# Kernel tuning notes

Measured on AMD Instinct MI355X. Metric: run time of the kernel, lower is better.

## Reference

```python
import jax, jax.numpy as jnp
import numpy as np
import math

L, D_T, D, NL, NH, FFN, C, B = 24, 1024, 256, 12, 4, 1024, 2, 2048
HD = D // NH


def _layernorm(x, g, b, eps=1e-5):
    m = jnp.mean(x, axis=-1, keepdims=True)
    v = jnp.mean(jnp.square(x - m), axis=-1, keepdims=True)
    return (x - m) * jax.lax.rsqrt(v + eps) * g + b


def _rotate_half(x):
    x1, x2 = jnp.split(x, 2, axis=-1)
    return jnp.concatenate([-x2, x1], axis=-1)


def setup_inputs() -> dict:
    key = jax.random.key(0)
    ks = iter(jax.random.split(key, 64))
    n = lambda shape, s=0.02: jax.random.normal(next(ks), shape, dtype=jnp.float32) * s
    inp = {}
    inp['teacher_cls'] = jax.random.normal(next(ks), (B, L, D_T), dtype=jnp.float32)
    # input LN + projection
    inp['in_ln_g'] = jnp.ones((D_T,), jnp.float32); inp['in_ln_b'] = jnp.zeros((D_T,), jnp.float32)
    inp['proj_w'] = n((D, D_T)); inp['proj_b'] = jnp.zeros((D,), jnp.float32)
    # RoPE caches (buffers)
    inv_freq = 1.0 / (10000.0 ** (np.arange(0, D, 2, dtype=np.float32) / D))
    t = np.arange(L, dtype=np.float32)
    freqs = np.einsum('i,j->ij', t, inv_freq)
    emb = np.concatenate([freqs, freqs], axis=-1)
    inp['cos_cached'] = jnp.asarray(np.cos(emb)[None])  # [1,L,D]
    inp['sin_cached'] = jnp.asarray(np.sin(emb)[None])
    inp['pre_ln_g'] = jnp.ones((D,), jnp.float32); inp['pre_ln_b'] = jnp.zeros((D,), jnp.float32)
    # stacked transformer layer params [NL, ...]
    inp['l_ln1_g'] = jnp.ones((NL, D), jnp.float32); inp['l_ln1_b'] = jnp.zeros((NL, D), jnp.float32)
    inp['l_inw'] = n((NL, 3 * D, D)); inp['l_inb'] = jnp.zeros((NL, 3 * D), jnp.float32)
    inp['l_outw'] = n((NL, D, D)); inp['l_outb'] = jnp.zeros((NL, D), jnp.float32)
    inp['l_ln2_g'] = jnp.ones((NL, D), jnp.float32); inp['l_ln2_b'] = jnp.zeros((NL, D), jnp.float32)
    inp['l_w12'] = n((NL, 2 * FFN, D)); inp['l_b12'] = jnp.zeros((NL, 2 * FFN), jnp.float32)
    inp['l_w3'] = n((NL, D, FFN)); inp['l_b3'] = jnp.zeros((NL, D), jnp.float32)
    inp['post_ln_g'] = jnp.ones((D,), jnp.float32); inp['post_ln_b'] = jnp.zeros((D,), jnp.float32)
    # entropy gate
    inp['eg_w1'] = n((L, D, 8), 0.01); inp['eg_b1'] = jnp.zeros((L, 8), jnp.float32)
    inp['eg_w2'] = n((L, 8, 1), 0.01); inp['eg_b2'] = jnp.zeros((L, 1), jnp.float32)
    # per-position heads (stacked)
    inp['halt_w'] = n((L, D + 1)); inp['halt_b'] = jnp.full((L,), -4.0, jnp.float32)
    inp['cls_w'] = n((L, C, D)); inp['cls_b'] = jnp.zeros((L, C), jnp.float32)
    return inp


def _mha(x, inw, inb, outw, outb, mask):
    Bb, Ll, Dd = x.shape
    qkv = x @ inw.T + inb                              # [B,L,3D]
    q, k, v = jnp.split(qkv, 3, axis=-1)
    def heads(t):
        return t.reshape(Bb, Ll, NH, HD).transpose(0, 2, 1, 3)  # [B,H,L,hd]
    q, k, v = heads(q), heads(k), heads(v)
    scores = jnp.einsum('bhqd,bhkd->bhqk', q, k) / math.sqrt(HD)
    scores = jnp.where(mask, -jnp.inf, scores)
    attn = jax.nn.softmax(scores, axis=-1)
    o = jnp.einsum('bhqk,bhkd->bhqd', attn, v)
    o = o.transpose(0, 2, 1, 3).reshape(Bb, Ll, Dd)
    return o @ outw.T + outb


def reference(teacher_cls, in_ln_g, in_ln_b, proj_w, proj_b, cos_cached, sin_cached,
              pre_ln_g, pre_ln_b, l_ln1_g, l_ln1_b, l_inw, l_inb, l_outw, l_outb,
              l_ln2_g, l_ln2_b, l_w12, l_b12, l_w3, l_b3, post_ln_g, post_ln_b,
              eg_w1, eg_b1, eg_w2, eg_b2, halt_w, halt_b, cls_w, cls_b):
    x = _layernorm(teacher_cls, in_ln_g, in_ln_b)
    x = x @ proj_w.T + proj_b                          # [B,L,D]
    x = x * cos_cached + _rotate_half(x) * sin_cached  # RoPE
    z = _layernorm(x, pre_ln_g, pre_ln_b)
    mask = jnp.triu(jnp.ones((L, L), bool), 1)         # causal
    for i in range(NL):
        xn = _layernorm(z, l_ln1_g[i], l_ln1_b[i])
        z = z + _mha(xn, l_inw[i], l_inb[i], l_outw[i], l_outb[i], mask)
        xn = _layernorm(z, l_ln2_g[i], l_ln2_b[i])
        w12_out = xn @ l_w12[i].T + l_b12[i]           # [B,L,2*FFN]
        x1, x2 = jnp.split(w12_out, 2, axis=-1)
        hidden = jax.nn.silu(x1) * x2
        z = z + hidden @ l_w3[i].T + l_b3[i]
    z = _layernorm(z, post_ln_g, post_ln_b)
    # batched per-position classifier heads
    class_logits = jnp.einsum('bld,lcd->blc', z, cls_w) + cls_b   # [B,L,C]
    log_probs = jax.nn.log_softmax(class_logits, axis=-1)
    probs = jnp.exp(log_probs)
    probs_safe = jnp.clip(probs, 1e-10, 1.0)
    ent = -jnp.sum(probs_safe * jnp.log(probs_safe), axis=-1, keepdims=True)
    ent_norm = jnp.clip(ent / math.log(C), 0.0, 1.0)              # [B,L,1]
    # entropy gate
    h = jnp.tanh(jnp.einsum('bld,ldh->blh', z, eg_w1) + eg_b1)
    gate = jax.nn.sigmoid(jnp.einsum('blh,lho->blo', h, eg_w2) + eg_b2)
    gated = ent_norm * gate                                        # [B,L,1]
    # batched per-position halting heads
    combined = jnp.concatenate([z, gated], axis=-1)                # [B,L,D+1]
    halting_logits = jnp.einsum('bld,ld->bl', combined, halt_w) + halt_b
    return (halting_logits, class_logits, z)
```

## Files before the change

### kernel.cpp

```cpp
#include <hip/hip_runtime.h>
#include <hip/hip_bf16.h>
#include <math.h>

#define L_SEQ 24
#define DT 1024
#define DM 256
#define NLAYER 12
#define NHEAD 4
#define HDIM 64
#define FFND 1024
#define NCLS 2
#define NBATCH 2048
#define NTOK (NBATCH*L_SEQ)

typedef float f32x4 __attribute__((ext_vector_type(4)));
typedef __bf16 bf16x4 __attribute__((ext_vector_type(4)));
typedef __bf16 bf16x8 __attribute__((ext_vector_type(8)));

#define GLDS16(gp, lp) __builtin_amdgcn_global_load_lds((const __attribute__((address_space(1))) void*)(gp), (__attribute__((address_space(3))) void*)(lp), 16, 0, 0)
#define VMWAIT(N) asm volatile("s_waitcnt vmcnt(" #N ")" ::: "memory")
#define LGKM0()   asm volatile("s_waitcnt lgkmcnt(0)" ::: "memory")

__device__ inline float wred_sum(float v){
#pragma unroll
  for (int o = 32; o > 0; o >>= 1) v += __shfl_xor(v, o);
  return v;
}
__device__ inline float wred_max(float v){
#pragma unroll
  for (int o = 32; o > 0; o >>= 1) v = fmaxf(v, __shfl_xor(v, o));
  return v;
}

__device__ __forceinline__ void stage16x32(const __bf16* __restrict__ g, int ldk, int k0,
                                           __bf16* ldsbase, int lane, int rowbase){
  int r = rowbase + (lane >> 2);
  int cs = (lane & 3) ^ ((lane >> 3) & 3);
  GLDS16(g + (size_t)r*ldk + k0 + cs*8, ldsbase);
}
__device__ __forceinline__ bf16x8 frag32(const __bf16* tile, int row, int lane){
  int p = (lane >> 4) ^ ((row >> 1) & 3);
  return *(const bf16x8*)(tile + (row << 5) + (p << 3));
}

__device__ __forceinline__ int xcd_work(){
  int nwg = gridDim.x, bid = blockIdx.x;
  return (bid & 7) * (nwg >> 3) + (bid >> 3);
}

__global__ void cvt_all_kernel(const float* __restrict__ a0, __bf16* __restrict__ o0, int n0,
                               const float* __restrict__ a1, __bf16* __restrict__ o1, int n1,
                               const float* __restrict__ a2, __bf16* __restrict__ o2, int n2,
                               const float* __restrict__ a3, __bf16* __restrict__ o3, int n3,
                               const float* __restrict__ a4, __bf16* __restrict__ o4, int n4){
  int stride = gridDim.x * blockDim.x;
  int i0 = blockIdx.x * blockDim.x + threadIdx.x;
  const float* as[5] = {a0,a1,a2,a3,a4};
  __bf16* os[5] = {o0,o1,o2,o3,o4};
  int ns[5] = {n0,n1,n2,n3,n4};
#pragma unroll
  for (int s = 0; s < 5; s++){
    const float* a = as[s]; __bf16* o = os[s]; int n = ns[s];
    for (int i = i0; i < n; i += stride){
      float4 v = ((const float4*)a)[i];
      bf16x4 ov;
      ov[0] = (__bf16)v.x; ov[1] = (__bf16)v.y; ov[2] = (__bf16)v.z; ov[3] = (__bf16)v.w;
      ((bf16x4*)o)[i] = ov;
    }
  }
}

__global__ __launch_bounds__(256) void ln1024_kernel(
    const float* __restrict__ in, const float* __restrict__ g, const float* __restrict__ bb,
    __bf16* __restrict__ out){
  int row = blockIdx.x;
  int tid = threadIdx.x, wid = tid >> 6, lane = tid & 63;
  float4 x = ((const float4*)(in + (size_t)row*DT))[tid];
  float s = x.x + x.y + x.z + x.w;
  float q = x.x*x.x + x.y*x.y + x.z*x.z + x.w*x.w;
  s = wred_sum(s); q = wred_sum(q);
  __shared__ float red[8];
  if (lane == 0){ red[wid] = s; red[4+wid] = q; }
  __syncthreads();
  s = red[0]+red[1]+red[2]+red[3];
  q = red[4]+red[5]+red[6]+red[7];
  float mean = s * (1.f/DT);
  float rstd = rsqrtf(q*(1.f/DT) - mean*mean + 1e-5f);
  float4 gv = ((const float4*)g)[tid], bv = ((const float4*)bb)[tid];
  bf16x4 o;
  o[0] = (__bf16)((x.x-mean)*rstd*gv.x + bv.x);
  o[1] = (__bf16)((x.y-mean)*rstd*gv.y + bv.y);
  o[2] = (__bf16)((x.z-mean)*rstd*gv.z + bv.z);
  o[3] = (__bf16)((x.w-mean)*rstd*gv.w + bv.w);
  ((bf16x4*)(out + (size_t)row*DT))[tid] = o;
}

__global__ __launch_bounds__(256) void rope_preln_kernel(
    float* __restrict__ z, const float* __restrict__ cosc, const float* __restrict__ sinc,
    const float* __restrict__ g, const float* __restrict__ bb,
    const float* __restrict__ g1, const float* __restrict__ b1, __bf16* __restrict__ xnb){
  int row = blockIdx.x*4 + (threadIdx.x >> 6);
  int lane = threadIdx.x & 63;
  int l = row % L_SEQ;
  float4 x = ((const float4*)(z + (size_t)row*DM))[lane];
  float4 p;
  p.x = __shfl_xor(x.x, 32); p.y = __shfl_xor(x.y, 32);
  p.z = __shfl_xor(x.z, 32); p.w = __shfl_xor(x.w, 32);
  float sgn = (lane < 32) ? -1.f : 1.f;
  float4 c = ((const float4*)(cosc + l*DM))[lane];
  float4 sn = ((const float4*)(sinc + l*DM))[lane];
  float4 xr;
  xr.x = x.x*c.x + sgn*p.x*sn.x;
  xr.y = x.y*c.y + sgn*p.y*sn.y;
  xr.z = x.z*c.z + sgn*p.z*sn.z;
  xr.w = x.w*c.w + sgn*p.w*sn.w;
  float s = wred_sum(xr.x + xr.y + xr.z + xr.w);
  float q = wred_sum(xr.x*xr.x + xr.y*xr.y + xr.z*xr.z + xr.w*xr.w);
  float mean = s * (1.f/DM);
  float rstd = rsqrtf(q*(1.f/DM) - mean*mean + 1e-5f);
  float4 gv = ((const float4*)g)[lane], bv = ((const float4*)bb)[lane];
  float4 y;
  y.x = (xr.x-mean)*rstd*gv.x + bv.x;
  y.y = (xr.y-mean)*rstd*gv.y + bv.y;
  y.z = (xr.z-mean)*rstd*gv.z + bv.z;
  y.w = (xr.w-mean)*rstd*gv.w + bv.w;
  ((float4*)(z + (size_t)row*DM))[lane] = y;
  float s2 = wred_sum(y.x + y.y + y.z + y.w);
  float q2 = wred_sum(y.x*y.x + y.y*y.y + y.z*y.z + y.w*y.w);
  float mean2 = s2 * (1.f/DM);
  float rstd2 = rsqrtf(q2*(1.f/DM) - mean2*mean2 + 1e-5f);
  float4 g1v = ((const float4*)g1)[lane], b1v = ((const float4*)b1)[lane];
  bf16x4 o;
  o[0] = (__bf16)((y.x-mean2)*rstd2*g1v.x + b1v.x);
  o[1] = (__bf16)((y.y-mean2)*rstd2*g1v.y + b1v.y);
  o[2] = (__bf16)((y.z-mean2)*rstd2*g1v.z + b1v.z);
  o[3] = (__bf16)((y.w-mean2)*rstd2*g1v.w + b1v.w);
  ((bf16x4*)(xnb + (size_t)row*DM))[lane] = o;
}

template<int MODE, int K>
__global__ __launch_bounds__(512) void gemm512_kernel(
    const __bf16* __restrict__ A, const __bf16* __restrict__ W,
    const float* __restrict__ bias,
    float* __restrict__ Cf, __bf16* __restrict__ Cb,
    int N, int nt){
  __shared__ __align__(16) __bf16 As[2][256*32];
  __shared__ __align__(16) __bf16 Bs[2][256*32];
  int work = xcd_work();
  int bm = work / nt, bn = work % nt;
  int wid = threadIdx.x >> 6, lane = threadIdx.x & 63;
  int wr = wid >> 1, wc = wid & 1;
  int li = lane & 15, g4 = (lane >> 4) << 2;
  f32x4 acc[8][4] = {};
  const __bf16* ga = A + (size_t)bm*256*K;
  const __bf16* gb = W + (size_t)bn*256*K;
  const int NT = K/32;
  auto STAGE = [&](int b, int t){
    int k0 = t*32;
    if (wid < 4){
#pragma unroll
      for (int j = 0; j < 4; j++){ int r = (wid*4 + j)*16; stage16x32(ga, K, k0, &As[b][r<<5], lane, r); }
    } else {
#pragma unroll
      for (int j = 0; j < 4; j++){ int r = ((wid-4)*4 + j)*16; stage16x32(gb, K, k0, &Bs[b][r<<5], lane, r); }
    }
  };
  STAGE(0, 0);
  STAGE(1, 1);
  int cur = 0;
  for (int t = 0; t < NT; t++){
    if (t + 1 < NT) { VMWAIT(4); } else { VMWAIT(0); }
    __builtin_amdgcn_s_barrier();
    bf16x8 xf[4], wf[8];
#pragma unroll
    for (int mi = 0; mi < 4; mi++) xf[mi] = frag32(As[cur], wr*64 + mi*16 + li, lane);
#pragma unroll
    for (int ni = 0; ni < 8; ni++) wf[ni] = frag32(Bs[cur], wc*128 + ni*16 + li, lane);
    LGKM0();
    __builtin_amdgcn_sched_barrier(0);
    __builtin_amdgcn_s_barrier();
    if (t + 2 < NT) STAGE(cur, t+2);
    __builtin_amdgcn_s_setprio(1);
#pragma unroll
    for (int ni = 0; ni < 8; ni++)
#pragma unroll
      for (int mi = 0; mi < 4; mi++)
        acc[ni][mi] = __builtin_amdgcn_mfma_f32_16x16x32_bf16(wf[ni], xf[mi], acc[ni][mi], 0, 0, 0);
    __builtin_amdgcn_s_setprio(0);
    cur ^= 1;
  }
#pragma unroll
  for (int mi = 0; mi < 4; mi++){
    int m = bm*256 + wr*64 + mi*16 + li;
#pragma unroll
    for (int ni = 0; ni < 8; ni++){
      int n = bn*256 + wc*128 + ni*16 + g4;
      f32x4 bv = *(const f32x4*)(bias + n);
      f32x4 o = acc[ni][mi] + bv;
      if (MODE == 0){
        *(f32x4*)(Cf + (size_t)m*N + n) = o;
      } else {
        bf16x4 ob;
        ob[0] = (__bf16)o[0]; ob[1] = (__bf16)o[1]; ob[2] = (__bf16)o[2]; ob[3] = (__bf16)o[3];
        *(bf16x4*)(Cb + (size_t)m*N + n) = ob;
      }
    }
  }
}

__global__ __launch_bounds__(512) void gemm_glu_kernel(
    const __bf16* __restrict__ A, const __bf16* __restrict__ W12,
    const float* __restrict__ bias, __bf16* __restrict__ H){
  __shared__ __align__(16) __bf16 As[8][192*32];
  __shared__ __align__(16) __bf16 B1s[2][128*32];
  __shared__ __align__(16) __bf16 B2s[2][128*32];
  const int K = 256;
  int bm = xcd_work();
  int wid = threadIdx.x >> 6, lane = threadIdx.x & 63;
  int wr = wid >> 1, wc = wid & 1;
  int li = lane & 15, g4 = (lane >> 4) << 2;
  const __bf16* ga = A + (size_t)bm*192*K;
#pragma unroll
  for (int j = 0; j < 12; j++){
    int g = j*8 + wid;
    int chunk = g / 12, u = g % 12;
    stage16x32(ga, K, chunk*32, &As[chunk][(u*16) << 5], lane, u*16);
  }
  auto STAGEB = [&](int buf, int g){
    int bn = g >> 3, k0 = (g & 7)*32;
    const __bf16* gb1 = W12 + (size_t)bn*128*K;
    stage16x32(gb1,              K, k0, &B1s[buf][(wid*16) << 5], lane, wid*16);
    stage16x32(gb1 + (size_t)1024*K, K, k0, &B2s[buf][(wid*16) << 5], lane, wid*16);
  };
  STAGEB(0, 0);
  STAGEB(1, 1);
  f32x4 acc1[4][3] = {}, acc2[4][3] = {};
  int cur = 0;
  for (int g = 0; g < 64; g++){
    int k = g & 7, bn = g >> 3;
    if (g == 0)            { VMWAIT(2);  }
    else if (g == 63)      { VMWAIT(0);  }
    else if (k == 0)       { VMWAIT(14); }
    else                   { VMWAIT(2);  }
    __builtin_amdgcn_s_barrier();
    bf16x8 xf[3], w1f[4], w2f[4];
#pragma unroll
    for (int mi = 0; mi < 3; mi++) xf[mi] = frag32(As[k], wr*48 + mi*16 + li, lane);
#pragma unroll
    for (int ni = 0; ni < 4; ni++){
      w1f[ni] = frag32(B1s[cur], wc*64 + ni*16 + li, lane);
      w2f[ni] = frag32(B2s[cur], wc*64 + ni*16 + li, lane);
    }
    LGKM0();
    __builtin_amdgcn_sched_barrier(0);
    __builtin_amdgcn_s_barrier();
    if (g + 2 < 64) STAGEB(cur, g + 2);
    __builtin_amdgcn_s_setprio(1);
#pragma unroll
    for (int ni = 0; ni < 4; ni++)
#pragma unroll
      for (int mi = 0; mi < 3; mi++){
        acc1[ni][mi] = __builtin_amdgcn_mfma_f32_16x16x32_bf16(w1f[ni], xf[mi], acc1[ni][mi], 0, 0, 0);
        acc2[ni][mi] = __builtin_amdgcn_mfma_f32_16x16x32_bf16(w2f[ni], xf[mi], acc2[ni][mi], 0, 0, 0);
      }
    __builtin_amdgcn_s_setprio(0);
    cur ^= 1;
    if (k == 7){
#pragma unroll
      for (int mi = 0; mi < 3; mi++){
        int m = bm*192 + wr*48 + mi*16 + li;
#pragma unroll
        for (int ni = 0; ni < 4; ni++){
          int n = bn*128 + wc*64 + ni*16 + g4;
          f32x4 b1v = *(const f32x4*)(bias + n);
          f32x4 b2v = *(const f32x4*)(bias + 1024 + n);
          bf16x4 ob;
#pragma unroll
          for (int r = 0; r < 4; r++){
            float v1 = acc1[ni][mi][r] + b1v[r];
            float v2 = acc2[ni][mi][r] + b2v[r];
            float sig = 1.f/(1.f + __expf(-v1));
            ob[r] = (__bf16)(v1*sig*v2);
          }
          *(bf16x4*)(H + (size_t)m*FFND + n) = ob;
          acc1[ni][mi] = (f32x4)(0.f);
          acc2[ni][mi] = (f32x4)(0.f);
        }
      }
    }
  }
}

template<int K>
__global__ __launch_bounds__(512) void gemm_ln_kernel(
    const __bf16* __restrict__ A, const __bf16* __restrict__ W,
    const float* __restrict__ bias, float* __restrict__ z,
    const float* __restrict__ lng, const float* __restrict__ lnb,
    __bf16* __restrict__ outb, float* __restrict__ outf){
  __shared__ __align__(16) __bf16 As[2][256*32];
  __shared__ __align__(16) __bf16 Bs[2][256*32];
  __shared__ float redS[256][2], redQ[256][2];
  int bm = xcd_work();
  int wid = threadIdx.x >> 6, lane = threadIdx.x & 63;
  int wr = wid >> 1, wc = wid & 1;
  int li = lane & 15, g4 = (lane >> 4) << 2;
  f32x4 acc[8][4] = {};
  const __bf16* ga = A + (size_t)bm*256*K;
  const int NT = K/32;
  auto STAGE = [&](int b, int t){
    int k0 = t*32;
    if (wid < 4){
#pragma unroll
      for (int j = 0; j < 4; j++){ int r = (wid*4 + j)*16; stage16x32(ga, K, k0, &As[b][r<<5], lane, r); }
    } else {
#pragma unroll
      for (int j = 0; j < 4; j++){ int r = ((wid-4)*4 + j)*16; stage16x32(W, K, k0, &Bs[b][r<<5], lane, r); }
    }
  };
  STAGE(0, 0);
  STAGE(1, 1);
  int cur = 0;
  for (int t = 0; t < NT; t++){
    if (t + 1 < NT) { VMWAIT(4); } else { VMWAIT(0); }
    __builtin_amdgcn_s_barrier();
    bf16x8 xf[4], wf[8];
#pragma unroll
    for (int mi = 0; mi < 4; mi++) xf[mi] = frag32(As[cur], wr*64 + mi*16 + li, lane);
#pragma unroll
    for (int ni = 0; ni < 8; ni++) wf[ni] = frag32(Bs[cur], wc*128 + ni*16 + li, lane);
    LGKM0();
    __builtin_amdgcn_sched_barrier(0);
    __builtin_amdgcn_s_barrier();
    if (t + 2 < NT) STAGE(cur, t+2);
    __builtin_amdgcn_s_setprio(1);
#pragma unroll
    for (int ni = 0; ni < 8; ni++)
#pragma unroll
      for (int mi = 0; mi < 4; mi++)
        acc[ni][mi] = __builtin_amdgcn_mfma_f32_16x16x32_bf16(wf[ni], xf[mi], acc[ni][mi], 0, 0, 0);
    __builtin_amdgcn_s_setprio(0);
    cur ^= 1;
  }
  float sA[4] = {}, qA[4] = {};
#pragma unroll
  for (int mi = 0; mi < 4; mi++){
    int m = bm*256 + wr*64 + mi*16 + li;
#pragma unroll
    for (int ni = 0; ni < 8; ni++){
      int n = wc*128 + ni*16 + g4;
      f32x4 zv = *(const f32x4*)(z + (size_t)m*DM + n);
      f32x4 bv = *(const f32x4*)(bias + n);
      f32x4 v = acc[ni][mi] + bv + zv;
      acc[ni][mi] = v;
      *(f32x4*)(z + (size_t)m*DM + n) = v;
#pragma unroll
      for (int r = 0; r < 4; r++){ sA[mi] += v[r]; qA[mi] += v[r]*v[r]; }
    }
  }
  __syncthreads();
#pragma unroll
  for (int mi = 0; mi < 4; mi++){
    float s = sA[mi], q = qA[mi];
    s += __shfl_xor(s, 16); q += __shfl_xor(q, 16);
    s += __shfl_xor(s, 32); q += __shfl_xor(q, 32);
    if (lane < 16){ redS[wr*64 + mi*16 + li][wc] = s; redQ[wr*64 + mi*16 + li][wc] = q; }
  }
  __syncthreads();
#pragma unroll
  for (int mi = 0; mi < 4; mi++){
    int ml = wr*64 + mi*16 + li;
    float s = redS[ml][0] + redS[ml][1];
    float q = redQ[ml][0] + redQ[ml][1];
    float mean = s * (1.f/DM);
    float rstd = rsqrtf(q*(1.f/DM) - mean*mean + 1e-5f);
    int m = bm*256 + ml;
#pragma unroll
    for (int ni = 0; ni < 8; ni++){
      int n = wc*128 + ni*16 + g4;
      f32x4 gv = *(const f32x4*)(lng + n);
      f32x4 bv = *(const f32x4*)(lnb + n);
      if (outb){
        bf16x4 o;
#pragma unroll
        for (int r = 0; r < 4; r++) o[r] = (__bf16)((acc[ni][mi][r] - mean)*rstd*gv[r] + bv[r]);
        *(bf16x4*)(outb + (size_t)m*DM + n) = o;
      } else {
        f32x4 o;
#pragma unroll
        for (int r = 0; r < 4; r++) o[r] = (acc[ni][mi][r] - mean)*rstd*gv[r] + bv[r];
        *(f32x4*)(outf + (size_t)m*DM + n) = o;
      }
    }
  }
}

__global__ __launch_bounds__(256) void attn_kernel(const __bf16* __restrict__ qkv, __bf16* __restrict__ ob){
  int b = blockIdx.x;
  int h = threadIdx.x >> 6, lane = threadIdx.x & 63;
  __shared__ __align__(16) __bf16 Qs[NHEAD][L_SEQ][HDIM];
  __shared__ __align__(16) __bf16 Ks[NHEAD][L_SEQ][HDIM];
  __shared__ float Ps[NHEAD][L_SEQ][L_SEQ];
  const __bf16* base = qkv + (size_t)b*L_SEQ*768;
  float V[L_SEQ];
#pragma unroll
  for (int t = 0; t < L_SEQ; t++){
    int sw = lane ^ ((t & 7) << 3);
    Qs[h][t][sw] = base[t*768 + h*64 + lane];
    Ks[h][t][sw] = base[t*768 + 256 + h*64 + lane];
    V[t] = (float)base[t*768 + 512 + h*64 + lane];
  }
  __syncthreads();
  for (int p = lane; p < L_SEQ*L_SEQ; p += 64){
    int q = p / L_SEQ, k = p - q*L_SEQ;
    if (k <= q){
      int qx = (q & 7) << 3, kx = (k & 7) << 3;
      const __bf16* qr = Qs[h][q];
      const __bf16* kr = Ks[h][k];
      float s = 0.f;
#pragma unroll
      for (int d = 0; d < 64; d += 4){
        bf16x4 qa = *(const bf16x4*)(qr + (d ^ qx));
        bf16x4 ka = *(const bf16x4*)(kr + (d ^ kx));
        s += (float)qa[0]*(float)ka[0] + (float)qa[1]*(float)ka[1]
           + (float)qa[2]*(float)ka[2] + (float)qa[3]*(float)ka[3];
      }
      Ps[h][q][k] = s * 0.125f;
    }
  }
  __syncthreads();
  for (int q = 0; q < L_SEQ; q++){
    float v = (lane <= q) ? Ps[h][q][lane] : -1e30f;
    float mx = wred_max(v);
    float e = (lane <= q) ? __expf(v - mx) : 0.f;
    float sm = wred_sum(e);
    if (lane < L_SEQ) Ps[h][q][lane] = e / sm;
  }
  __syncthreads();
  for (int q = 0; q < L_SEQ; q++){
    float o = 0.f;
    for (int k = 0; k <= q; k++) o += Ps[h][q][k] * V[k];
    ob[((size_t)b*L_SEQ + q)*DM + h*64 + lane] = (__bf16)o;
  }
}

__global__ __launch_bounds__(256) void heads_kernel(
    const float* __restrict__ z,
    const float* __restrict__ cls_w, const float* __restrict__ cls_b,
    const float* __restrict__ eg_w1, const float* __restrict__ eg_b1,
    const float* __restrict__ eg_w2, const float* __restrict__ eg_b2,
    const float* __restrict__ halt_w, const float* __restrict__ halt_b,
    float* __restrict__ halt_out, float* __restrict__ cls_out){
  int m = blockIdx.x*4 + (threadIdx.x >> 6);
  int lane = threadIdx.x & 63;
  int l = m % L_SEQ;
  float4 zv = ((const float4*)(z + (size_t)m*DM))[lane];
  float4 w0 = ((const float4*)(cls_w + ((size_t)l*2 + 0)*DM))[lane];
  float4 w1 = ((const float4*)(cls_w + ((size_t)l*2 + 1)*DM))[lane];
  float c0 = wred_sum(zv.x*w0.x + zv.y*w0.y + zv.z*w0.z + zv.w*w0.w) + cls_b[l*2 + 0];
  float c1 = wred_sum(zv.x*w1.x + zv.y*w1.y + zv.z*w1.z + zv.w*w1.w) + cls_b[l*2 + 1];
  float mx = fmaxf(c0, c1);
  float e0 = __expf(c0 - mx), e1 = __expf(c1 - mx);
  float inv = 1.f/(e0 + e1);
  float p0 = fminf(fmaxf(e0*inv, 1e-10f), 1.f);
  float p1 = fminf(fmaxf(e1*inv, 1e-10f), 1.f);
  float ent = -(p0*__logf(p0) + p1*__logf(p1));
  float entn = fminf(fmaxf(ent * 1.44269504f, 0.f), 1.f);
  const float4* wg = (const float4*)(eg_w1 + ((size_t)l*DM + 4*lane)*8);
  float hacc[8] = {};
#pragma unroll
  for (int dd = 0; dd < 4; dd++){
    float zd = (dd==0) ? zv.x : (dd==1) ? zv.y : (dd==2) ? zv.z : zv.w;
    float4 a = wg[dd*2], b = wg[dd*2 + 1];
    hacc[0] += zd*a.x; hacc[1] += zd*a.y; hacc[2] += zd*a.z; hacc[3] += zd*a.w;
    hacc[4] += zd*b.x; hacc[5] += zd*b.y; hacc[6] += zd*b.z; hacc[7] += zd*b.w;
  }
  float gin = 0.f;
#pragma unroll
  for (int j = 0; j < 8; j++){
    float hj = wred_sum(hacc[j]);
    hj = tanhf(hj + eg_b1[l*8 + j]);
    gin += hj * eg_w2[l*8 + j];
  }
  gin += eg_b2[l];
  float gate = 1.f/(1.f + __expf(-gin));
  float gated = entn * gate;
  const float* hw = halt_w + (size_t)l*257;
  float hp = zv.x*hw[4*lane] + zv.y*hw[4*lane+1] + zv.z*hw[4*lane+2] + zv.w*hw[4*lane+3];
  float hl = wred_sum(hp) + gated*hw[256] + halt_b[l];
  if (lane == 0) halt_out[m] = hl;
  if (lane < 2) cls_out[(size_t)m*2 + lane] = lane ? c1 : c0;
}

extern "C" void kernel_launch(void* const* d_in, const int* in_sizes, int n_in,
                              void* d_out, int out_size, void* d_ws, size_t ws_size,
                              hipStream_t stream){
  const float* teacher = (const float*)d_in[0];
  const float* in_ln_g = (const float*)d_in[1];
  const float* in_ln_b = (const float*)d_in[2];
  const float* proj_w  = (const float*)d_in[3];
  const float* proj_b  = (const float*)d_in[4];
  const float* cosc    = (const float*)d_in[5];
  const float* sinc    = (const float*)d_in[6];
  const float* pre_g   = (const float*)d_in[7];
  const float* pre_b   = (const float*)d_in[8];
  const float* l_ln1_g = (const float*)d_in[9];
  const float* l_ln1_b = (const float*)d_in[10];
  const float* l_inw   = (const float*)d_in[11];
  const float* l_inb   = (const float*)d_in[12];
  const float* l_outw  = (const float*)d_in[13];
  const float* l_outb  = (const float*)d_in[14];
  const float* l_ln2_g = (const float*)d_in[15];
  const float* l_ln2_b = (const float*)d_in[16];
  const float* l_w12   = (const float*)d_in[17];
  const float* l_b12   = (const float*)d_in[18];
  const float* l_w3    = (const float*)d_in[19];
  const float* l_b3    = (const float*)d_in[20];
  const float* post_g  = (const float*)d_in[21];
  const float* post_b  = (const float*)d_in[22];
  const float* eg_w1   = (const float*)d_in[23];
  const float* eg_b1   = (const float*)d_in[24];
  const float* eg_w2   = (const float*)d_in[25];
  const float* eg_b2   = (const float*)d_in[26];
  const float* halt_w  = (const float*)d_in[27];
  const float* halt_b  = (const float*)d_in[28];
  const float* cls_w   = (const float*)d_in[29];
  const float* cls_b   = (const float*)d_in[30];

  float* out = (float*)d_out;
  float* halt_out = out;
  float* cls_out  = out + NTOK;
  float* z_out    = out + NTOK + (size_t)NTOK*NCLS;

  char* ws = (char*)d_ws;
  size_t off = 0;
  auto alloc = [&](size_t bytes){ void* p = ws + off; off += (bytes + 255) & ~(size_t)255; return p; };
  float*  zbuf = (float*) alloc((size_t)NTOK*DM*4);
  __bf16* xnb  = (__bf16*)alloc((size_t)NTOK*DM*2);
  __bf16* qkvb = (__bf16*)alloc((size_t)NTOK*768*2);
  __bf16* obuf = (__bf16*)alloc((size_t)NTOK*DM*2);
  __bf16* bigb = (__bf16*)alloc((size_t)NTOK*1024*2);
  __bf16* w_proj = (__bf16*)alloc((size_t)262144*2);
  __bf16* w_in   = (__bf16*)alloc((size_t)2359296*2);
  __bf16* w_out  = (__bf16*)alloc((size_t)786432*2);
  __bf16* w_12   = (__bf16*)alloc((size_t)6291456*2);
  __bf16* w_3    = (__bf16*)alloc((size_t)3145728*2);

  cvt_all_kernel<<<2048, 256, 0, stream>>>(proj_w, w_proj, 262144/4,
                                           l_inw, w_in, 2359296/4,
                                           l_outw, w_out, 786432/4,
                                           l_w12, w_12, 6291456/4,
                                           l_w3, w_3, 3145728/4);

  ln1024_kernel<<<NTOK, 256, 0, stream>>>(teacher, in_ln_g, in_ln_b, bigb);
  gemm512_kernel<0, 1024><<<192, 512, 0, stream>>>(bigb, w_proj, proj_b, zbuf, nullptr, 256, 1);
  rope_preln_kernel<<<NTOK/4, 256, 0, stream>>>(zbuf, cosc, sinc, pre_g, pre_b, l_ln1_g, l_ln1_b, xnb);

  for (int i = 0; i < NLAYER; i++){
    gemm512_kernel<1, 256><<<576, 512, 0, stream>>>(xnb, w_in + (size_t)i*768*256, l_inb + i*768, nullptr, qkvb, 768, 3);
    attn_kernel<<<NBATCH, 256, 0, stream>>>(qkvb, obuf);
    gemm_ln_kernel<256><<<192, 512, 0, stream>>>(obuf, w_out + (size_t)i*256*256, l_outb + i*256,
                                                 zbuf, l_ln2_g + i*256, l_ln2_b + i*256, xnb, nullptr);
    gemm_glu_kernel<<<256, 512, 0, stream>>>(xnb, w_12 + (size_t)i*2048*256, l_b12 + i*2048, bigb);
    bool last = (i == NLAYER-1);
    gemm_ln_kernel<1024><<<192, 512, 0, stream>>>(bigb, w_3 + (size_t)i*256*1024, l_b3 + i*256,
                                                  zbuf,
                                                  last ? post_g : l_ln1_g + (i+1)*256,
                                                  last ? post_b : l_ln1_b + (i+1)*256,
                                                  last ? nullptr : xnb,
                                                  last ? z_out : nullptr);
  }

  heads_kernel<<<NTOK/4, 256, 0, stream>>>(z_out, cls_w, cls_b, eg_w1, eg_b1, eg_w2, eg_b2,
                                           halt_w, halt_b, halt_out, cls_out);
}
```

Before: 4.143 ms.

## Fuse SwiGLU up-projection and down-projection with LayerNorm into one FFN kernel

Replaces the separate GLU GEMM and W3 GEMM+LN kernels with a single kernel. Each 192-row block computes 64-column slices of the SwiGLU hidden state, keeps them in LDS, and feeds them straight into the W3 accumulation, followed by the residual add and LayerNorm. This removes the round trip of the bf16 hidden activation (NTOK x 1024) through global memory and one launch per layer. The cost is that the W3 MFMAs now run with only 256 blocks, there are many more barriers, W12/W3 tiles are re-staged with shallow prefetch, register pressure rises from the 8x3 accumulator, and xcd_work scheduling is replaced by plain blockIdx.

```diff
diff --git a/kernel.cpp b/kernel.cpp
--- a/kernel.cpp
+++ b/kernel.cpp
@@ -208,89 +208,6 @@
   }
 }
 
-__global__ __launch_bounds__(512) void gemm_glu_kernel(
-    const __bf16* __restrict__ A, const __bf16* __restrict__ W12,
-    const float* __restrict__ bias, __bf16* __restrict__ H){
-  __shared__ __align__(16) __bf16 As[8][192*32];
-  __shared__ __align__(16) __bf16 B1s[2][128*32];
-  __shared__ __align__(16) __bf16 B2s[2][128*32];
-  const int K = 256;
-  int bm = xcd_work();
-  int wid = threadIdx.x >> 6, lane = threadIdx.x & 63;
-  int wr = wid >> 1, wc = wid & 1;
-  int li = lane & 15, g4 = (lane >> 4) << 2;
-  const __bf16* ga = A + (size_t)bm*192*K;
-#pragma unroll
-  for (int j = 0; j < 12; j++){
-    int g = j*8 + wid;
-    int chunk = g / 12, u = g % 12;
-    stage16x32(ga, K, chunk*32, &As[chunk][(u*16) << 5], lane, u*16);
-  }
-  auto STAGEB = [&](int buf, int g){
-    int bn = g >> 3, k0 = (g & 7)*32;
-    const __bf16* gb1 = W12 + (size_t)bn*128*K;
-    stage16x32(gb1,              K, k0, &B1s[buf][(wid*16) << 5], lane, wid*16);
-    stage16x32(gb1 + (size_t)1024*K, K, k0, &B2s[buf][(wid*16) << 5], lane, wid*16);
-  };
-  STAGEB(0, 0);
-  STAGEB(1, 1);
-  f32x4 acc1[4][3] = {}, acc2[4][3] = {};
-  int cur = 0;
-  for (int g = 0; g < 64; g++){
-    int k = g & 7, bn = g >> 3;
-    if (g == 0)            { VMWAIT(2);  }
-    else if (g == 63)      { VMWAIT(0);  }
-    else if (k == 0)       { VMWAIT(14); }
-    else                   { VMWAIT(2);  }
-    __builtin_amdgcn_s_barrier();
-    bf16x8 xf[3], w1f[4], w2f[4];
-#pragma unroll
-    for (int mi = 0; mi < 3; mi++) xf[mi] = frag32(As[k], wr*48 + mi*16 + li, lane);
-#pragma unroll
-    for (int ni = 0; ni < 4; ni++){
-      w1f[ni] = frag32(B1s[cur], wc*64 + ni*16 + li, lane);
-      w2f[ni] = frag32(B2s[cur], wc*64 + ni*16 + li, lane);
-    }
-    LGKM0();
-    __builtin_amdgcn_sched_barrier(0);
-    __builtin_amdgcn_s_barrier();
-    if (g + 2 < 64) STAGEB(cur, g + 2);
-    __builtin_amdgcn_s_setprio(1);
-#pragma unroll
-    for (int ni = 0; ni < 4; ni++)
-#pragma unroll
-      for (int mi = 0; mi < 3; mi++){
-        acc1[ni][mi] = __builtin_amdgcn_mfma_f32_16x16x32_bf16(w1f[ni], xf[mi], acc1[ni][mi], 0, 0, 0);
-        acc2[ni][mi] = __builtin_amdgcn_mfma_f32_16x16x32_bf16(w2f[ni], xf[mi], acc2[ni][mi], 0, 0, 0);
-      }
-    __builtin_amdgcn_s_setprio(0);
-    cur ^= 1;
-    if (k == 7){
-#pragma unroll
-      for (int mi = 0; mi < 3; mi++){
-        int m = bm*192 + wr*48 + mi*16 + li;
-#pragma unroll
-        for (int ni = 0; ni < 4; ni++){
-          int n = bn*128 + wc*64 + ni*16 + g4;
-          f32x4 b1v = *(const f32x4*)(bias + n);
-          f32x4 b2v = *(const f32x4*)(bias + 1024 + n);
-          bf16x4 ob;
-#pragma unroll
-          for (int r = 0; r < 4; r++){
-            float v1 = acc1[ni][mi][r] + b1v[r];
-            float v2 = acc2[ni][mi][r] + b2v[r];
-            float sig = 1.f/(1.f + __expf(-v1));
-            ob[r] = (__bf16)(v1*sig*v2);
-          }
-          *(bf16x4*)(H + (size_t)m*FFND + n) = ob;
-          acc1[ni][mi] = (f32x4)(0.f);
-          acc2[ni][mi] = (f32x4)(0.f);
-        }
-      }
-    }
-  }
-}
-
 template<int K>
 __global__ __launch_bounds__(512) void gemm_ln_kernel(
     const __bf16* __restrict__ A, const __bf16* __restrict__ W,
@@ -388,6 +305,181 @@
         f32x4 o;
 #pragma unroll
         for (int r = 0; r < 4; r++) o[r] = (acc[ni][mi][r] - mean)*rstd*gv[r] + bv[r];
+        *(f32x4*)(outf + (size_t)m*DM + n) = o;
+      }
+    }
+  }
+}
+
+__global__ __launch_bounds__(512) void gemm_ffn_kernel(
+    const __bf16* __restrict__ A, const __bf16* __restrict__ W12,
+    const float* __restrict__ b12, const __bf16* __restrict__ W3,
+    const float* __restrict__ b3, float* __restrict__ z,
+    const float* __restrict__ lng, const float* __restrict__ lnb,
+    __bf16* __restrict__ outb, float* __restrict__ outf){
+  __shared__ __align__(16) __bf16 As[8][192*32];
+  __shared__ __align__(16) __bf16 Wb[3][128*32];
+  __shared__ __align__(16) __bf16 Hb[192*32];
+  __shared__ __align__(16) __bf16 W3b[256*32];
+  float* redS = (float*)&Wb[0][0];
+  float* redQ = redS + 384;
+  int bm = blockIdx.x;
+  int wid = threadIdx.x >> 6, lane = threadIdx.x & 63;
+  int wr = wid >> 1, wc = wid & 1;
+  int li = lane & 15, g4 = (lane >> 4) << 2;
+  const __bf16* ga = A + (size_t)bm*192*256;
+
+  auto STAGE_W3 = [&](int bn, int kc){
+#pragma unroll
+    for (int j = 0; j < 2; j++){
+      int u = j*8 + wid;
+      stage16x32(W3, 1024, bn*64 + kc*32, &W3b[(u*16) << 5], lane, u*16);
+    }
+  };
+  auto STAGE_W12 = [&](int buf, int bn, int c){
+    const __bf16* src = W12 + ((wid < 4) ? (size_t)(bn*64 + wid*16)*256
+                                         : (size_t)(1024 + bn*64 + (wid-4)*16)*256);
+    stage16x32(src, 256, c*32, &Wb[buf][(wid*16) << 5], lane, 0);
+  };
+#pragma unroll
+  for (int j = 0; j < 12; j++){
+    int u = j*8 + wid;
+    int c = u / 12, rj = u % 12;
+    stage16x32(ga, 256, c*32, &As[c][(rj*16) << 5], lane, rj*16);
+  }
+  STAGE_W3(0, 0);
+  STAGE_W12(0, 0, 0);
+  STAGE_W12(1, 0, 1);
+  STAGE_W12(2, 0, 2);
+
+  f32x4 Cacc[8][3] = {};
+  for (int bn = 0; bn < 16; bn++){
+    f32x4 a1[2][3] = {}, a2[2][3] = {};
+    for (int s = 0; s < 8; s++){
+      if (s < 6) { VMWAIT(2); } else if (s == 6) { VMWAIT(1); } else { VMWAIT(0); }
+      __builtin_amdgcn_s_barrier();
+      bf16x8 xf[3], w1f[2], w2f[2];
+      const __bf16* wbuf = Wb[s % 3];
+#pragma unroll
+      for (int mi = 0; mi < 3; mi++) xf[mi] = frag32(As[s], wr*48 + mi*16 + li, lane);
+#pragma unroll
+      for (int ni = 0; ni < 2; ni++){
+        w1f[ni] = frag32(wbuf, wc*32 + ni*16 + li, lane);
+        w2f[ni] = frag32(wbuf, 64 + wc*32 + ni*16 + li, lane);
+      }
+      LGKM0();
+      __builtin_amdgcn_sched_barrier(0);
+      __builtin_amdgcn_s_barrier();
+      if (s <= 4) STAGE_W12(s % 3, bn, s + 3);
+      __builtin_amdgcn_s_setprio(1);
+#pragma unroll
+      for (int ni = 0; ni < 2; ni++)
+#pragma unroll
+        for (int mi = 0; mi < 3; mi++){
+          a1[ni][mi] = __builtin_amdgcn_mfma_f32_16x16x32_bf16(w1f[ni], xf[mi], a1[ni][mi], 0, 0, 0);
+          a2[ni][mi] = __builtin_amdgcn_mfma_f32_16x16x32_bf16(w2f[ni], xf[mi], a2[ni][mi], 0, 0, 0);
+        }
+      __builtin_amdgcn_s_setprio(0);
+    }
+    for (int kc = 0; kc < 2; kc++){
+      if (wc == kc){
+#pragma unroll
+        for (int ni = 0; ni < 2; ni++){
+          int cl0 = ni*16 + g4;
+          int ncol = bn*64 + kc*32 + cl0;
+          f32x4 b1v = *(const f32x4*)(b12 + ncol);
+          f32x4 b2v = *(const f32x4*)(b12 + 1024 + ncol);
+#pragma unroll
+          for (int mi = 0; mi < 3; mi++){
+            int m = wr*48 + mi*16 + li;
+            bf16x4 hv;
+#pragma unroll
+            for (int r = 0; r < 4; r++){
+              float v1 = a1[ni][mi][r] + b1v[r];
+              float v2 = a2[ni][mi][r] + b2v[r];
+              float sig = 1.f/(1.f + __expf(-v1));
+              hv[r] = (__bf16)(v1*sig*v2);
+            }
+            int p = (cl0 >> 3) ^ ((m >> 1) & 3);
+            *(bf16x4*)((char*)Hb + m*64 + p*16 + (cl0 & 7)*2) = hv;
+          }
+        }
+      }
+      LGKM0();
+      if (kc == 1) { VMWAIT(0); }
+      __builtin_amdgcn_s_barrier();
+      bf16x8 hf[3], w3f[8];
+#pragma unroll
+      for (int mi = 0; mi < 3; mi++) hf[mi] = frag32(Hb, wr*48 + mi*16 + li, lane);
+#pragma unroll
+      for (int ni = 0; ni < 8; ni++) w3f[ni] = frag32(W3b, wc*128 + ni*16 + li, lane);
+      LGKM0();
+      __builtin_amdgcn_sched_barrier(0);
+      __builtin_amdgcn_s_barrier();
+      if (kc == 0){
+        STAGE_W3(bn, 1);
+      } else if (bn < 15){
+        STAGE_W3(bn + 1, 0);
+        STAGE_W12(0, bn + 1, 0);
+        STAGE_W12(1, bn + 1, 1);
+        STAGE_W12(2, bn + 1, 2);
+      }
+      __builtin_amdgcn_s_setprio(1);
+#pragma unroll
+      for (int ni = 0; ni < 8; ni++)
+#pragma unroll
+        for (int mi = 0; mi < 3; mi++)
+          Cacc[ni][mi] = __builtin_amdgcn_mfma_f32_16x16x32_bf16(w3f[ni], hf[mi], Cacc[ni][mi], 0, 0, 0);
+      __builtin_amdgcn_s_setprio(0);
+    }
+  }
+  __syncthreads();
+  float sA[3] = {}, qA[3] = {};
+#pragma unroll
+  for (int mi = 0; mi < 3; mi++){
+    int m = bm*192 + wr*48 + mi*16 + li;
+#pragma unroll
+    for (int ni = 0; ni < 8; ni++){
+      int n = wc*128 + ni*16 + g4;
+      f32x4 zv = *(const f32x4*)(z + (size_t)m*DM + n);
+      f32x4 bv = *(const f32x4*)(b3 + n);
+      f32x4 v = Cacc[ni][mi] + bv + zv;
+      Cacc[ni][mi] = v;
+      *(f32x4*)(z + (size_t)m*DM + n) = v;
+#pragma unroll
+      for (int r = 0; r < 4; r++){ sA[mi] += v[r]; qA[mi] += v[r]*v[r]; }
+    }
+  }
+#pragma unroll
+  for (int mi = 0; mi < 3; mi++){
+    float s = sA[mi], q = qA[mi];
+    s += __shfl_xor(s, 16); q += __shfl_xor(q, 16);
+    s += __shfl_xor(s, 32); q += __shfl_xor(q, 32);
+    if (lane < 16){ int rl = wr*48 + mi*16 + li; redS[rl*2 + wc] = s; redQ[rl*2 + wc] = q; }
+  }
+  __syncthreads();
+#pragma unroll
+  for (int mi = 0; mi < 3; mi++){
+    int rl = wr*48 + mi*16 + li;
+    float s = redS[rl*2 + 0] + redS[rl*2 + 1];
+    float q = redQ[rl*2 + 0] + redQ[rl*2 + 1];
+    float mean = s * (1.f/DM);
+    float rstd = rsqrtf(q*(1.f/DM) - mean*mean + 1e-5f);
+    int m = bm*192 + rl;
+#pragma unroll
+    for (int ni = 0; ni < 8; ni++){
+      int n = wc*128 + ni*16 + g4;
+      f32x4 gv = *(const f32x4*)(lng + n);
+      f32x4 bv = *(const f32x4*)(lnb + n);
+      if (outb){
+        bf16x4 o;
+#pragma unroll
+        for (int r = 0; r < 4; r++) o[r] = (__bf16)((Cacc[ni][mi][r] - mean)*rstd*gv[r] + bv[r]);
+        *(bf16x4*)(outb + (size_t)m*DM + n) = o;
+      } else {
+        f32x4 o;
+#pragma unroll
+        for (int r = 0; r < 4; r++) o[r] = (Cacc[ni][mi][r] - mean)*rstd*gv[r] + bv[r];
         *(f32x4*)(outf + (size_t)m*DM + n) = o;
       }
     }
@@ -560,14 +652,13 @@
     attn_kernel<<<NBATCH, 256, 0, stream>>>(qkvb, obuf);
     gemm_ln_kernel<256><<<192, 512, 0, stream>>>(obuf, w_out + (size_t)i*256*256, l_outb + i*256,
                                                  zbuf, l_ln2_g + i*256, l_ln2_b + i*256, xnb, nullptr);
-    gemm_glu_kernel<<<256, 512, 0, stream>>>(xnb, w_12 + (size_t)i*2048*256, l_b12 + i*2048, bigb);
     bool last = (i == NLAYER-1);
-    gemm_ln_kernel<1024><<<192, 512, 0, stream>>>(bigb, w_3 + (size_t)i*256*1024, l_b3 + i*256,
-                                                  zbuf,
-                                                  last ? post_g : l_ln1_g + (i+1)*256,
-                                                  last ? post_b : l_ln1_b + (i+1)*256,
-                                                  last ? nullptr : xnb,
-                                                  last ? z_out : nullptr);
+    gemm_ffn_kernel<<<256, 512, 0, stream>>>(xnb, w_12 + (size_t)i*2048*256, l_b12 + i*2048,
+                                             w_3 + (size_t)i*256*1024, l_b3 + i*256, zbuf,
+                                             last ? post_g : l_ln1_g + (i+1)*256,
+                                             last ? post_b : l_ln1_b + (i+1)*256,
+                                             last ? nullptr : xnb,
+                                             last ? z_out : nullptr);
   }
 
   heads_kernel<<<NTOK/4, 256, 0, stream>>>(z_out, cls_w, cls_b, eg_w1, eg_b1, eg_w2, eg_b2,
```

Result: faster. 4.045 ms (-2.4%).

## Retile GLU GEMM into 256x128 tiles and shrink LN-GEMM row tiles to 192

Applied to the files above, without the earlier changes.

The GLU GEMM no longer keeps a whole 192-row A block resident while looping over all output columns. Each workgroup now processes three 256x128 output tiles, streaming both A and the two weight halves through double-buffered LDS, and loads the bias once per tile. The residual+LayerNorm GEMMs drop from 256-row to 192-row tiles, which raises their grid from 192 to 256 blocks. Both kernels get more blocks and better CU balance on the 256-CU part, in exchange for re-reading A more often in the GLU kernel and more complex vmcnt bookkeeping.

```diff
diff --git a/kernel.cpp b/kernel.cpp
--- a/kernel.cpp
+++ b/kernel.cpp
@@ -211,41 +211,48 @@
 __global__ __launch_bounds__(512) void gemm_glu_kernel(
     const __bf16* __restrict__ A, const __bf16* __restrict__ W12,
     const float* __restrict__ bias, __bf16* __restrict__ H){
-  __shared__ __align__(16) __bf16 As[8][192*32];
+  __shared__ __align__(16) __bf16 As[2][256*32];
   __shared__ __align__(16) __bf16 B1s[2][128*32];
   __shared__ __align__(16) __bf16 B2s[2][128*32];
   const int K = 256;
-  int bm = xcd_work();
+  int work = xcd_work();
   int wid = threadIdx.x >> 6, lane = threadIdx.x & 63;
   int wr = wid >> 1, wc = wid & 1;
   int li = lane & 15, g4 = (lane >> 4) << 2;
-  const __bf16* ga = A + (size_t)bm*192*K;
-#pragma unroll
-  for (int j = 0; j < 12; j++){
-    int g = j*8 + wid;
-    int chunk = g / 12, u = g % 12;
-    stage16x32(ga, K, chunk*32, &As[chunk][(u*16) << 5], lane, u*16);
-  }
-  auto STAGEB = [&](int buf, int g){
-    int bn = g >> 3, k0 = (g & 7)*32;
-    const __bf16* gb1 = W12 + (size_t)bn*128*K;
-    stage16x32(gb1,              K, k0, &B1s[buf][(wid*16) << 5], lane, wid*16);
-    stage16x32(gb1 + (size_t)1024*K, K, k0, &B2s[buf][(wid*16) << 5], lane, wid*16);
+  f32x4 acc1[4][4] = {}, acc2[4][4] = {};
+  f32x4 B1v[4], B2v[4];
+  auto STAGE = [&](int buf, int g){
+    int T = work*3 + (g >> 3);
+    int bmT = T >> 3, bnT = T & 7;
+    int k0 = (g & 7)*32;
+    const __bf16* ga  = A   + (size_t)bmT*256*K;
+    const __bf16* gb1 = W12 + (size_t)bnT*128*K;
+    const __bf16* gb2 = gb1 + (size_t)1024*K;
+    if (wid < 4){
+#pragma unroll
+      for (int j = 0; j < 4; j++){ int r = (wid*4 + j)*16; stage16x32(ga, K, k0, &As[buf][r<<5], lane, r); }
+    } else if (wid < 6){
+#pragma unroll
+      for (int j = 0; j < 4; j++){ int r = ((wid-4)*4 + j)*16; stage16x32(gb1, K, k0, &B1s[buf][r<<5], lane, r); }
+    } else {
+#pragma unroll
+      for (int j = 0; j < 4; j++){ int r = ((wid-6)*4 + j)*16; stage16x32(gb2, K, k0, &B2s[buf][r<<5], lane, r); }
+    }
   };
-  STAGEB(0, 0);
-  STAGEB(1, 1);
-  f32x4 acc1[4][3] = {}, acc2[4][3] = {};
+  STAGE(0, 0);
+  STAGE(1, 1);
   int cur = 0;
-  for (int g = 0; g < 64; g++){
-    int k = g & 7, bn = g >> 3;
-    if (g == 0)            { VMWAIT(2);  }
-    else if (g == 63)      { VMWAIT(0);  }
-    else if (k == 0)       { VMWAIT(14); }
-    else                   { VMWAIT(2);  }
+  for (int g = 0; g < 24; g++){
+    int k = g & 7;
+    if (g == 23)      { VMWAIT(0); }
+    else if (k == 0)  { if (g) { VMWAIT(20); } else { VMWAIT(4); } }
+    else if (k == 1)  { if (g == 1) { VMWAIT(12); } else { VMWAIT(28); } }
+    else if (k == 2)  { VMWAIT(12); }
+    else              { VMWAIT(4); }
     __builtin_amdgcn_s_barrier();
-    bf16x8 xf[3], w1f[4], w2f[4];
-#pragma unroll
-    for (int mi = 0; mi < 3; mi++) xf[mi] = frag32(As[k], wr*48 + mi*16 + li, lane);
+    bf16x8 xf[4], w1f[4], w2f[4];
+#pragma unroll
+    for (int mi = 0; mi < 4; mi++) xf[mi] = frag32(As[cur], wr*64 + mi*16 + li, lane);
 #pragma unroll
     for (int ni = 0; ni < 4; ni++){
       w1f[ni] = frag32(B1s[cur], wc*64 + ni*16 + li, lane);
@@ -254,31 +261,43 @@
     LGKM0();
     __builtin_amdgcn_sched_barrier(0);
     __builtin_amdgcn_s_barrier();
-    if (g + 2 < 64) STAGEB(cur, g + 2);
+    if (g + 2 < 24) STAGE(cur, g + 2);
+    __builtin_amdgcn_sched_barrier(0);
+    if (k == 0){
+      int bnT = (work*3 + (g >> 3)) & 7;
+#pragma unroll
+      for (int ni = 0; ni < 4; ni++){
+        int n = bnT*128 + wc*64 + ni*16 + g4;
+        B1v[ni] = *(const f32x4*)(bias + n);
+        B2v[ni] = *(const f32x4*)(bias + 1024 + n);
+      }
+      __builtin_amdgcn_sched_barrier(0);
+    }
     __builtin_amdgcn_s_setprio(1);
 #pragma unroll
     for (int ni = 0; ni < 4; ni++)
 #pragma unroll
-      for (int mi = 0; mi < 3; mi++){
+      for (int mi = 0; mi < 4; mi++){
         acc1[ni][mi] = __builtin_amdgcn_mfma_f32_16x16x32_bf16(w1f[ni], xf[mi], acc1[ni][mi], 0, 0, 0);
         acc2[ni][mi] = __builtin_amdgcn_mfma_f32_16x16x32_bf16(w2f[ni], xf[mi], acc2[ni][mi], 0, 0, 0);
       }
     __builtin_amdgcn_s_setprio(0);
     cur ^= 1;
     if (k == 7){
-#pragma unroll
-      for (int mi = 0; mi < 3; mi++){
-        int m = bm*192 + wr*48 + mi*16 + li;
+      __builtin_amdgcn_sched_barrier(0);
+      int T = work*3 + (g >> 3);
+      int bmT = T >> 3, bnT = T & 7;
+#pragma unroll
+      for (int mi = 0; mi < 4; mi++){
+        int m = bmT*256 + wr*64 + mi*16 + li;
 #pragma unroll
         for (int ni = 0; ni < 4; ni++){
-          int n = bn*128 + wc*64 + ni*16 + g4;
-          f32x4 b1v = *(const f32x4*)(bias + n);
-          f32x4 b2v = *(const f32x4*)(bias + 1024 + n);
+          int n = bnT*128 + wc*64 + ni*16 + g4;
           bf16x4 ob;
 #pragma unroll
           for (int r = 0; r < 4; r++){
-            float v1 = acc1[ni][mi][r] + b1v[r];
-            float v2 = acc2[ni][mi][r] + b2v[r];
+            float v1 = acc1[ni][mi][r] + B1v[ni][r];
+            float v2 = acc2[ni][mi][r] + B2v[ni][r];
             float sig = 1.f/(1.f + __expf(-v1));
             ob[r] = (__bf16)(v1*sig*v2);
           }
@@ -287,6 +306,7 @@
           acc2[ni][mi] = (f32x4)(0.f);
         }
       }
+      __builtin_amdgcn_sched_barrier(0);
     }
   }
 }
@@ -297,21 +317,21 @@
     const float* __restrict__ bias, float* __restrict__ z,
     const float* __restrict__ lng, const float* __restrict__ lnb,
     __bf16* __restrict__ outb, float* __restrict__ outf){
-  __shared__ __align__(16) __bf16 As[2][256*32];
+  __shared__ __align__(16) __bf16 As[2][192*32];
   __shared__ __align__(16) __bf16 Bs[2][256*32];
-  __shared__ float redS[256][2], redQ[256][2];
+  __shared__ float redS[192][2], redQ[192][2];
   int bm = xcd_work();
   int wid = threadIdx.x >> 6, lane = threadIdx.x & 63;
   int wr = wid >> 1, wc = wid & 1;
   int li = lane & 15, g4 = (lane >> 4) << 2;
-  f32x4 acc[8][4] = {};
-  const __bf16* ga = A + (size_t)bm*256*K;
+  f32x4 acc[8][3] = {};
+  const __bf16* ga = A + (size_t)bm*192*K;
   const int NT = K/32;
   auto STAGE = [&](int b, int t){
     int k0 = t*32;
     if (wid < 4){
 #pragma unroll
-      for (int j = 0; j < 4; j++){ int r = (wid*4 + j)*16; stage16x32(ga, K, k0, &As[b][r<<5], lane, r); }
+      for (int j = 0; j < 3; j++){ int r = (wid*3 + j)*16; stage16x32(ga, K, k0, &As[b][r<<5], lane, r); }
     } else {
 #pragma unroll
       for (int j = 0; j < 4; j++){ int r = ((wid-4)*4 + j)*16; stage16x32(W, K, k0, &Bs[b][r<<5], lane, r); }
@@ -321,11 +341,11 @@
   STAGE(1, 1);
   int cur = 0;
   for (int t = 0; t < NT; t++){
-    if (t + 1 < NT) { VMWAIT(4); } else { VMWAIT(0); }
+    if (t + 1 < NT) { VMWAIT(3); } else { VMWAIT(0); }
     __builtin_amdgcn_s_barrier();
-    bf16x8 xf[4], wf[8];
-#pragma unroll
-    for (int mi = 0; mi < 4; mi++) xf[mi] = frag32(As[cur], wr*64 + mi*16 + li, lane);
+    bf16x8 xf[3], wf[8];
+#pragma unroll
+    for (int mi = 0; mi < 3; mi++) xf[mi] = frag32(As[cur], wr*48 + mi*16 + li, lane);
 #pragma unroll
     for (int ni = 0; ni < 8; ni++) wf[ni] = frag32(Bs[cur], wc*128 + ni*16 + li, lane);
     LGKM0();
@@ -336,15 +356,15 @@
 #pragma unroll
     for (int ni = 0; ni < 8; ni++)
 #pragma unroll
-      for (int mi = 0; mi < 4; mi++)
+      for (int mi = 0; mi < 3; mi++)
         acc[ni][mi] = __builtin_amdgcn_mfma_f32_16x16x32_bf16(wf[ni], xf[mi], acc[ni][mi], 0, 0, 0);
     __builtin_amdgcn_s_setprio(0);
     cur ^= 1;
   }
-  float sA[4] = {}, qA[4] = {};
-#pragma unroll
-  for (int mi = 0; mi < 4; mi++){
-    int m = bm*256 + wr*64 + mi*16 + li;
+  float sA[3] = {}, qA[3] = {};
+#pragma unroll
+  for (int mi = 0; mi < 3; mi++){
+    int m = bm*192 + wr*48 + mi*16 + li;
 #pragma unroll
     for (int ni = 0; ni < 8; ni++){
       int n = wc*128 + ni*16 + g4;
@@ -359,21 +379,21 @@
   }
   __syncthreads();
 #pragma unroll
-  for (int mi = 0; mi < 4; mi++){
+  for (int mi = 0; mi < 3; mi++){
     float s = sA[mi], q = qA[mi];
     s += __shfl_xor(s, 16); q += __shfl_xor(q, 16);
     s += __shfl_xor(s, 32); q += __shfl_xor(q, 32);
-    if (lane < 16){ redS[wr*64 + mi*16 + li][wc] = s; redQ[wr*64 + mi*16 + li][wc] = q; }
+    if (lane < 16){ redS[wr*48 + mi*16 + li][wc] = s; redQ[wr*48 + mi*16 + li][wc] = q; }
   }
   __syncthreads();
 #pragma unroll
-  for (int mi = 0; mi < 4; mi++){
-    int ml = wr*64 + mi*16 + li;
+  for (int mi = 0; mi < 3; mi++){
+    int ml = wr*48 + mi*16 + li;
     float s = redS[ml][0] + redS[ml][1];
     float q = redQ[ml][0] + redQ[ml][1];
     float mean = s * (1.f/DM);
     float rstd = rsqrtf(q*(1.f/DM) - mean*mean + 1e-5f);
-    int m = bm*256 + ml;
+    int m = bm*192 + ml;
 #pragma unroll
     for (int ni = 0; ni < 8; ni++){
       int n = wc*128 + ni*16 + g4;
@@ -558,11 +578,11 @@
   for (int i = 0; i < NLAYER; i++){
     gemm512_kernel<1, 256><<<576, 512, 0, stream>>>(xnb, w_in + (size_t)i*768*256, l_inb + i*768, nullptr, qkvb, 768, 3);
     attn_kernel<<<NBATCH, 256, 0, stream>>>(qkvb, obuf);
-    gemm_ln_kernel<256><<<192, 512, 0, stream>>>(obuf, w_out + (size_t)i*256*256, l_outb + i*256,
+    gemm_ln_kernel<256><<<256, 512, 0, stream>>>(obuf, w_out + (size_t)i*256*256, l_outb + i*256,
                                                  zbuf, l_ln2_g + i*256, l_ln2_b + i*256, xnb, nullptr);
-    gemm_glu_kernel<<<256, 512, 0, stream>>>(xnb, w_12 + (size_t)i*2048*256, l_b12 + i*2048, bigb);
+    gemm_glu_kernel<<<512, 512, 0, stream>>>(xnb, w_12 + (size_t)i*2048*256, l_b12 + i*2048, bigb);
     bool last = (i == NLAYER-1);
-    gemm_ln_kernel<1024><<<192, 512, 0, stream>>>(bigb, w_3 + (size_t)i*256*1024, l_b3 + i*256,
+    gemm_ln_kernel<1024><<<256, 512, 0, stream>>>(bigb, w_3 + (size_t)i*256*1024, l_b3 + i*256,
                                                   zbuf,
                                                   last ? post_g : l_ln1_g + (i+1)*256,
                                                   last ? post_b : l_ln1_b + (i+1)*256,
```

Result: faster. 3.928 ms (-5.2%).
